# Kernel optimization log

Hardware: AMD Instinct MI355X
Metric: run time of the kernel (lower is better)

The kernel has to match this reference:

```python
import jax, jax.numpy as jnp
import numpy as np
import itertools

# LeViT-style Attention config (matches init_kwargs)
DIM = 256
KD = 32          # key_dim
H = 8            # num_heads
AR = 4           # attn_ratio
RES = 14
N = RES * RES    # 196 tokens
D = AR * KD      # per-head value dim = 128
DH = D * H       # 1024
NHKD = KD * H    # 256
HID = DH + 2 * NHKD  # 1536 = qkv width
EPS = 1e-5
SCALE = KD ** -0.5
BATCH = 256


def _bias_idxs():
    # Same construction as the torch module: index into table of unique abs offsets.
    points = list(itertools.product(range(RES), range(RES)))
    offs = {}
    idxs = []
    for p1 in points:
        for p2 in points:
            o = (abs(p1[0] - p2[0]), abs(p1[1] - p2[1]))
            if o not in offs:
                offs[o] = len(offs)
            idxs.append(offs[o])
    return np.asarray(idxs, dtype=np.int32).reshape(N, N), len(offs)


def _bn(x, g, b):
    # BatchNorm1d in training mode over the flattened (B*N, F) batch dim.
    mu = x.mean(axis=0)
    var = jnp.var(x, axis=0)  # biased, as torch BN uses for normalization
    return (x - mu) * jax.lax.rsqrt(var + EPS) * g + b


def setup_inputs() -> dict:
    key = jax.random.key(0)
    ks = jax.random.split(key, 8)
    idxs_np, n_off = _bias_idxs()  # n_off == 196 for RES=14
    x = jax.random.normal(ks[0], (BATCH, N, DIM), dtype=jnp.float32)
    Wqkv = jax.random.normal(ks[1], (HID, DIM), dtype=jnp.float32) * 0.02
    g1 = 1.0 + 0.1 * jax.random.normal(ks[2], (HID,), dtype=jnp.float32)
    b1 = 0.1 * jax.random.normal(ks[3], (HID,), dtype=jnp.float32)
    # init is zeros in the module; use small randn so the bias path is exercised
    bias_table = 0.1 * jax.random.normal(ks[4], (H, n_off), dtype=jnp.float32)
    Wproj = jax.random.normal(ks[5], (DIM, DH), dtype=jnp.float32) * 0.02
    # bn_weight_init=0 in module; use nonzero so output/grads are nontrivial
    g2 = 1.0 + 0.1 * jax.random.normal(ks[6], (DIM,), dtype=jnp.float32)
    b2 = 0.1 * jax.random.normal(ks[7], (DIM,), dtype=jnp.float32)
    return {
        "x": x, "Wqkv": Wqkv, "g1": g1, "b1": b1,
        "bias_table": bias_table, "Wproj": Wproj, "g2": g2, "b2": b2,
        "idxs": jnp.asarray(idxs_np),
    }


def reference(x, Wqkv, g1, b1, bias_table, Wproj, g2, b2, idxs):
    B, Ntok, C = x.shape
    # qkv = Linear_BN(x): bias-free linear then BN over flattened (B*N, HID)
    h = jnp.einsum('bnc,hc->bnh', x, Wqkv)
    h = _bn(h.reshape(B * Ntok, HID), g1, b1).reshape(B, Ntok, H, -1)
    q = h[..., :KD].transpose(0, 2, 1, 3)            # (B,H,N,KD)
    k = h[..., KD:2 * KD].transpose(0, 2, 1, 3)      # (B,H,N,KD)
    v = h[..., 2 * KD:].transpose(0, 2, 1, 3)        # (B,H,N,D)
    bias = bias_table[:, idxs]                       # (H,N,N) relative-position bias gather
    attn = jnp.einsum('bhnd,bhmd->bhnm', q, k) * SCALE + bias
    attn = jax.nn.softmax(attn, axis=-1)
    o = jnp.einsum('bhnm,bhmd->bhnd', attn, v)
    o = o.transpose(0, 2, 1, 3).reshape(B, Ntok, DH)
    # proj = Hardswish -> Linear_BN(dh, dim)
    o = o * jnp.clip(o + 3.0, 0.0, 6.0) / 6.0
    o = jnp.einsum('bnd,cd->bnc', o, Wproj)
    o = _bn(o.reshape(B * Ntok, C), g2, b2).reshape(B, Ntok, C)
    return o
```

## Files before the change

kernel.cpp:

```cpp
#include <hip/hip_runtime.h>

typedef _Float16 f16;
typedef __attribute__((ext_vector_type(8))) _Float16 half8;
typedef __attribute__((ext_vector_type(4))) _Float16 half4;
typedef __attribute__((ext_vector_type(4))) float   f4;

#define NTOK   196
#define MROWS  50176
#define HIDN   1536
#define HPC    192
#define DHD    1024
#define EPSV   1e-5f
#define SCALEV 0.17677669529663687f

#define GLD16(gp, lp) __builtin_amdgcn_global_load_lds( \
    (const __attribute__((address_space(1))) unsigned int*)(gp), \
    (__attribute__((address_space(3))) unsigned int*)(lp), 16, 0, 0)

__device__ inline int swz8(int row) { return (((row & 7) ^ ((row >> 3) & 7))) * 8; }

__global__ void cvt_f32_f16(const float* __restrict__ src, f16* __restrict__ dst, int n4)
{
    int i = blockIdx.x * blockDim.x + threadIdx.x;
    if (i < n4) {
        float4 v = *(const float4*)&src[i * 4];
        half4 h = { (f16)v.x, (f16)v.y, (f16)v.z, (f16)v.w };
        *(half4*)&dst[i * 4] = h;
    }
}

__global__ void build_bias(const float* __restrict__ bt, const int* __restrict__ idxs,
                           f16* __restrict__ bf)
{
    int i = blockIdx.x * 256 + threadIdx.x;
    if (i >= 8 * 208 * 224) return;
    int k = i % 224, q = (i / 224) % 208, h = i / (224 * 208);
    float v = -30000.f;
    if (q < NTOK && k < NTOK) v = bt[h * NTOK + idxs[q * NTOK + k]];
    bf[i] = (f16)v;
}

#define PIPE_BODY(CA, CB, PA, PB, ST, HASPF, GATE)                              \
  {                                                                             \
    asm volatile("s_waitcnt vmcnt(" GATE ")" ::: "memory");                     \
    __builtin_amdgcn_s_barrier();                                               \
    __builtin_amdgcn_sched_barrier(0);                                          \
    if (HASPF) {                                                                \
      const f16* Apf_ = Ab + ((ST) + 2) * 32;                                   \
      const f16* Bpf_ = Bb + ((ST) + 2) * 32;                                   \
      GLD16(Apf_,          &PA[so0]);                                           \
      GLD16(Apf_ + 16 * K, &PA[so1]);                                           \
      GLD16(Bpf_,          &PB[so0]);                                           \
      GLD16(Bpf_ + 16 * K, &PB[so1]);                                           \
    }                                                                           \
    half8 a_[4], b_[4];                                                         \
    _Pragma("unroll")                                                           \
    for (int i_ = 0; i_ < 4; ++i_) {                                            \
      a_[i_] = *(const half8*)&CA[(wm + i_ * 16 + lm) * 32 + rs];               \
      b_[i_] = *(const half8*)&CB[(wn + i_ * 16 + lm) * 32 + rs];               \
    }                                                                           \
    asm volatile("s_waitcnt lgkmcnt(0)" ::: "memory");                          \
    __builtin_amdgcn_sched_barrier(0);                                          \
    _Pragma("unroll")                                                           \
    for (int i_ = 0; i_ < 4; ++i_)                                              \
      _Pragma("unroll")                                                         \
      for (int j_ = 0; j_ < 4; ++j_)                                            \
        acc[i_][j_] = __builtin_amdgcn_mfma_f32_16x16x32_f16(                   \
            a_[i_], b_[j_], acc[i_][j_], 0, 0, 0);                              \
  }

__global__ __launch_bounds__(256) void gemm1_qkv(
    const f16* __restrict__ A, const f16* __restrict__ B,
    f16* __restrict__ C, float* __restrict__ gsum, float* __restrict__ gsq)
{
    const int K = 256, ldc = HIDN;
    __shared__ f16 As0[4096], As1[4096], As2[4096];
    __shared__ f16 Bs0[4096], Bs1[4096], Bs2[4096];
    __shared__ float ssum[128], ssq[128];

    const int t = threadIdx.x;
    const int m0 = blockIdx.x * 128, n0 = blockIdx.y * 128;
    const int wid = t >> 6, lane = t & 63, quad = lane >> 4, lm = lane & 15;
    const int wm = (wid >> 1) * 64, wn = (wid & 1) * 64;

    const int lr = lane >> 2;
    const int lc = ((lane & 3) ^ (lr & 3)) * 8;
    const int so0 = (wid * 2 + 0) * 512, so1 = (wid * 2 + 1) * 512;
    const f16* Ab = A + (long)(m0 + wid * 32 + lr) * K + lc;
    const f16* Bb = B + (long)(n0 + wid * 32 + lr) * K + lc;
    const int rs = (quad ^ (lm & 3)) * 8;

    f4 acc[4][4] = {};

    GLD16(Ab,               &As0[so0]);
    GLD16(Ab + 16 * K,      &As0[so1]);
    GLD16(Bb,               &Bs0[so0]);
    GLD16(Bb + 16 * K,      &Bs0[so1]);
    GLD16(Ab + 32,          &As1[so0]);
    GLD16(Ab + 16 * K + 32, &As1[so1]);
    GLD16(Bb + 32,          &Bs1[so0]);
    GLD16(Bb + 16 * K + 32, &Bs1[so1]);

    PIPE_BODY(As0, Bs0, As2, Bs2, 0, 1, "4");
    PIPE_BODY(As1, Bs1, As0, Bs0, 1, 1, "4");
    PIPE_BODY(As2, Bs2, As1, Bs1, 2, 1, "4");
    PIPE_BODY(As0, Bs0, As2, Bs2, 3, 1, "4");
    PIPE_BODY(As1, Bs1, As0, Bs0, 4, 1, "4");
    PIPE_BODY(As2, Bs2, As1, Bs1, 5, 1, "4");
    PIPE_BODY(As0, Bs0, As2, Bs2, 6, 0, "4");
    PIPE_BODY(As1, Bs1, As0, Bs0, 7, 0, "0");

    __syncthreads();
    if (t < 128) { ssum[t] = 0.f; ssq[t] = 0.f; }
    __syncthreads();

    #pragma unroll
    for (int j = 0; j < 4; ++j) {
        int nl = wn + j*16 + lm;
        float psum = 0.f, psq = 0.f;
        #pragma unroll
        for (int i = 0; i < 4; ++i) {
            #pragma unroll
            for (int r = 0; r < 4; ++r) {
                int ml = wm + i*16 + quad*4 + r;
                float v = acc[i][j][r];
                f16 uh = (f16)v;
                float vb = (float)uh;
                C[(long)(m0 + ml) * ldc + n0 + nl] = uh;
                psum += vb; psq += vb * vb;
            }
        }
        atomicAdd(&ssum[nl], psum);
        atomicAdd(&ssq[nl], psq);
    }
    __syncthreads();
    if (t < 128) {
        atomicAdd(&gsum[n0 + t], ssum[t]);
        atomicAdd(&gsq[n0 + t],  ssq[t]);
    }
}

__global__ __launch_bounds__(256) void gemm2_proj(
    const f16* __restrict__ A, const f16* __restrict__ B,
    float* __restrict__ C, float* __restrict__ gsum, float* __restrict__ gsq)
{
    const int K = 1024, ldc = 256;
    __shared__ f16 As0[4096], As1[4096], As2[4096];
    __shared__ f16 Bs0[4096], Bs1[4096], Bs2[4096];
    __shared__ float ssum[128], ssq[128];

    const int t = threadIdx.x;
    const int m0 = blockIdx.x * 128, n0 = blockIdx.y * 128;
    const int wid = t >> 6, lane = t & 63, quad = lane >> 4, lm = lane & 15;
    const int wm = (wid >> 1) * 64, wn = (wid & 1) * 64;

    const int lr = lane >> 2;
    const int lc = ((lane & 3) ^ (lr & 3)) * 8;
    const int so0 = (wid * 2 + 0) * 512, so1 = (wid * 2 + 1) * 512;
    const f16* Ab = A + (long)(m0 + wid * 32 + lr) * K + lc;
    const f16* Bb = B + (long)(n0 + wid * 32 + lr) * K + lc;
    const int rs = (quad ^ (lm & 3)) * 8;

    f4 acc[4][4] = {};

    GLD16(Ab,               &As0[so0]);
    GLD16(Ab + 16 * K,      &As0[so1]);
    GLD16(Bb,               &Bs0[so0]);
    GLD16(Bb + 16 * K,      &Bs0[so1]);
    GLD16(Ab + 32,          &As1[so0]);
    GLD16(Ab + 16 * K + 32, &As1[so1]);
    GLD16(Bb + 32,          &Bs1[so0]);
    GLD16(Bb + 16 * K + 32, &Bs1[so1]);

    for (int s = 0; s < 30; s += 6) {
        PIPE_BODY(As0, Bs0, As2, Bs2, s + 0, 1, "4");
        PIPE_BODY(As1, Bs1, As0, Bs0, s + 1, 1, "4");
        PIPE_BODY(As2, Bs2, As1, Bs1, s + 2, 1, "4");
        PIPE_BODY(As0, Bs0, As2, Bs2, s + 3, 1, "4");
        PIPE_BODY(As1, Bs1, As0, Bs0, s + 4, 1, "4");
        PIPE_BODY(As2, Bs2, As1, Bs1, s + 5, 1, "4");
    }
    PIPE_BODY(As0, Bs0, As2, Bs2, 30, 0, "4");
    PIPE_BODY(As1, Bs1, As0, Bs0, 31, 0, "0");

    __syncthreads();
    if (t < 128) { ssum[t] = 0.f; ssq[t] = 0.f; }
    __syncthreads();

    #pragma unroll
    for (int j = 0; j < 4; ++j) {
        int nl = wn + j*16 + lm;
        float psum = 0.f, psq = 0.f;
        #pragma unroll
        for (int i = 0; i < 4; ++i) {
            #pragma unroll
            for (int r = 0; r < 4; ++r) {
                int ml = wm + i*16 + quad*4 + r;
                float v = acc[i][j][r];
                C[(long)(m0 + ml) * ldc + n0 + nl] = v;
                psum += v; psq += v * v;
            }
        }
        atomicAdd(&ssum[nl], psum);
        atomicAdd(&ssq[nl], psq);
    }
    __syncthreads();
    if (t < 128) {
        atomicAdd(&gsum[n0 + t], ssum[t]);
        atomicAdd(&gsq[n0 + t],  ssq[t]);
    }
}

__global__ void bn_fin(const float* __restrict__ gsum, const float* __restrict__ gsq,
                       const float* __restrict__ g, const float* __restrict__ b,
                       float* __restrict__ a_out, float* __restrict__ s_out, int nch)
{
    int c = blockIdx.x * blockDim.x + threadIdx.x;
    if (c >= nch) return;
    float inv  = 1.f / (float)MROWS;
    float mean = gsum[c] * inv;
    float var  = gsq[c] * inv - mean * mean;
    float a    = g[c] * rsqrtf(var + EPSV);
    a_out[c] = a;
    s_out[c] = b[c] - mean * a;
}

__global__ __launch_bounds__(832) void attn_kernel(
    const f16* __restrict__ hbuf, const float* __restrict__ a1, const float* __restrict__ s1,
    const f16* __restrict__ bf, f16* __restrict__ obuf)
{
    __shared__ f16   ks[208][32];
    __shared__ f16   vT[128][256];
    __shared__ float af[192], sf[192];

    const int t  = threadIdx.x;
    const int bb = blockIdx.x >> 3;
    const int hh = blockIdx.x & 7;
    const int wid = t >> 6, lane = t & 63, quad = lane >> 4, lm = lane & 15;

    if (t < 192) { af[t] = a1[hh * HPC + t]; sf[t] = s1[hh * HPC + t]; }
    half8 z8 = {};
    for (int i = t; i < 4096; i += 832) *(half8*)&vT[i >> 5][(i & 31) * 8] = z8;
    if (t < 384) ks[196 + (t >> 5)][t & 31] = (f16)0.f;
    __syncthreads();

    {
        int t8 = t & 7;
        for (int rr = t >> 3; rr < NTOK; rr += 104) {
            const f16* hrow = hbuf + (long)(bb * NTOK + rr) * HIDN + hh * HPC;
            int sr = swz8(rr);
            #pragma unroll
            for (int cc = 0; cc < 3; ++cc) {
                int cb = 32 + (t8 + cc * 8) * 8;
                if (cb >= 192) continue;
                half8 raw = *(const half8*)(hrow + cb);
                if (cb < 64) {
                    half8 ov;
                    #pragma unroll
                    for (int e = 0; e < 8; ++e)
                        ov[e] = (f16)((float)raw[e] * af[cb + e] + sf[cb + e]);
                    *(half8*)&ks[rr][(cb - 32 + sr) & 31] = ov;
                } else {
                    #pragma unroll
                    for (int e = 0; e < 8; ++e) {
                        int c = cb - 64 + e;
                        f16 ov = (f16)((float)raw[e] * af[cb + e] + sf[cb + e]);
                        vT[c][(rr + swz8(c)) & 255] = ov;
                    }
                }
            }
        }
    }
    __syncthreads();

    const int mt = wid;
    const int qrow = mt * 16 + lm;
    const f16* bfh = bf + hh * 208 * 224;

    long grow = (long)bb * NTOK + qrow;
    if (grow > (long)(MROWS - 1)) grow = MROWS - 1;
    half8 qraw = *(const half8*)(hbuf + grow * HIDN + hh * HPC + quad * 8);
    half8 qf;
    #pragma unroll
    for (int e = 0; e < 8; ++e)
        qf[e] = (f16)((float)qraw[e] * af[quad * 8 + e] + sf[quad * 8 + e]);

    f4 sreg[13];
    #pragma unroll
    for (int nt = 0; nt < 13; ++nt) {
        int krow = nt * 16 + lm;
        half8 ak = *(const half8*)&ks[krow][(quad * 8 + swz8(krow)) & 31];
        f4 z = {};
        sreg[nt] = __builtin_amdgcn_mfma_f32_16x16x32_f16(ak, qf, z, 0, 0, 0);
    }

    const f16* brow = bfh + qrow * 224 + quad * 4;
    float m = -3.0e38f;
    #pragma unroll
    for (int nt = 0; nt < 13; ++nt) {
        half4 b4 = *(const half4*)(brow + nt * 16);
        #pragma unroll
        for (int r = 0; r < 4; ++r) {
            sreg[nt][r] = fmaf(sreg[nt][r], SCALEV, (float)b4[r]);
            m = fmaxf(m, sreg[nt][r]);
        }
    }
    m = fmaxf(m, __shfl_xor(m, 16));
    m = fmaxf(m, __shfl_xor(m, 32));

    float s = 0.f;
    half4 ap[13];
    #pragma unroll
    for (int nt = 0; nt < 13; ++nt) {
        float e0 = __expf(sreg[nt][0] - m);
        float e1 = __expf(sreg[nt][1] - m);
        float e2 = __expf(sreg[nt][2] - m);
        float e3 = __expf(sreg[nt][3] - m);
        s += (e0 + e1) + (e2 + e3);
        ap[nt] = half4{ (f16)e0, (f16)e1, (f16)e2, (f16)e3 };
    }
    s += __shfl_xor(s, 16);
    s += __shfl_xor(s, 32);
    float rinv = 1.f / s;

    float rv[4];
    #pragma unroll
    for (int r = 0; r < 4; ++r) rv[r] = __shfl(rinv, quad * 4 + r);

    #pragma unroll
    for (int ct = 0; ct < 8; ++ct) {
        int c = ct * 16 + lm;
        int sc = swz8(c);
        f4 oa = {};
        #pragma unroll
        for (int nt = 0; nt < 13; ++nt) {
            half4 bv = *(const half4*)&vT[c][(nt * 16 + quad * 4 + sc) & 255];
            oa = __builtin_amdgcn_mfma_f32_16x16x16f16(ap[nt], bv, oa, 0, 0, 0);
        }
        #pragma unroll
        for (int r = 0; r < 4; ++r) {
            int qr = mt * 16 + quad * 4 + r;
            if (qr < 196) {
                float v  = oa[r] * rv[r];
                float hs = v * fminf(fmaxf(v + 3.f, 0.f), 6.f) * (1.f / 6.f);
                obuf[(long)(bb * NTOK + qr) * DHD + hh * 128 + c] = (f16)hs;
            }
        }
    }
}

__global__ __launch_bounds__(256) void bn_apply(
    float* __restrict__ out, const float* __restrict__ a2, const float* __restrict__ s2)
{
    __shared__ float aL[256], sL[256];
    int t = threadIdx.x;
    aL[t] = a2[t]; sL[t] = s2[t];
    __syncthreads();
    long total = (long)MROWS * 256 / 4;
    for (long i = (long)blockIdx.x * 256 + t; i < total; i += (long)gridDim.x * 256) {
        float4 v = *(float4*)&out[i * 4];
        int cb = (int)((i * 4) & 255);
        v.x = v.x * aL[cb + 0] + sL[cb + 0];
        v.y = v.y * aL[cb + 1] + sL[cb + 1];
        v.z = v.z * aL[cb + 2] + sL[cb + 2];
        v.w = v.w * aL[cb + 3] + sL[cb + 3];
        *(float4*)&out[i * 4] = v;
    }
}

extern "C" void kernel_launch(void* const* d_in, const int* in_sizes, int n_in,
                              void* d_out, int out_size, void* d_ws, size_t ws_size,
                              hipStream_t stream)
{
    (void)in_sizes; (void)n_in; (void)out_size; (void)ws_size;
    const float* x          = (const float*)d_in[0];
    const float* Wqkv       = (const float*)d_in[1];
    const float* g1         = (const float*)d_in[2];
    const float* b1         = (const float*)d_in[3];
    const float* bias_table = (const float*)d_in[4];
    const float* Wproj      = (const float*)d_in[5];
    const float* g2         = (const float*)d_in[6];
    const float* b2         = (const float*)d_in[7];
    const int*   idxs       = (const int*)d_in[8];
    float*       out        = (float*)d_out;

    char* ws = (char*)d_ws;
    f16* hbuf = (f16*)ws;
    f16* obuf = (f16*)(ws + 154140672LL);
    f16* xh   = (f16*)(ws + 154140672LL);
    f16* wqh  = (f16*)(ws + 154140672LL + 25690112LL);
    f16* wph  = (f16*)ws;
    float* stats = (float*)(ws + 256901120LL);
    float* gsum1 = stats;            float* gsq1 = stats + 1536;
    float* gsum2 = stats + 3072;     float* gsq2 = stats + 3328;
    float* a1 = stats + 3584;        float* s1 = a1 + 1536;
    float* a2 = s1 + 1536;           float* s2 = a2 + 256;
    f16* bias_full = (f16*)(ws + 256901120LL + 65536LL);

    hipMemsetAsync(stats, 0, 3584 * sizeof(float), stream);

    cvt_f32_f16<<<12544, 256, 0, stream>>>(x, xh, 3211264);
    cvt_f32_f16<<<384,   256, 0, stream>>>(Wqkv, wqh, 98304);
    build_bias<<<1456, 256, 0, stream>>>(bias_table, idxs, bias_full);

    gemm1_qkv<<<dim3(392, 12), 256, 0, stream>>>(xh, wqh, hbuf, gsum1, gsq1);
    bn_fin<<<6, 256, 0, stream>>>(gsum1, gsq1, g1, b1, a1, s1, 1536);

    attn_kernel<<<2048, 832, 0, stream>>>(hbuf, a1, s1, bias_full, obuf);

    cvt_f32_f16<<<256, 256, 0, stream>>>(Wproj, wph, 65536);

    gemm2_proj<<<dim3(392, 2), 256, 0, stream>>>(obuf, wph, out, gsum2, gsq2);
    bn_fin<<<1, 256, 0, stream>>>(gsum2, gsq2, g2, b2, a2, s2, 256);

    bn_apply<<<1024, 256, 0, stream>>>(out, a2, s2);
}
```

Before: 440.9 us.

## Use exp2 softmax with folded log2e, packed f16 BN affine, and MFMA setprio

```diff
diff --git a/kernel.cpp b/kernel.cpp
--- a/kernel.cpp
+++ b/kernel.cpp
@@ -11,7 +11,8 @@
 #define HPC    192
 #define DHD    1024
 #define EPSV   1e-5f
-#define SCALEV 0.17677669529663687f
+#define SCALE2 0.25503524f
+#define LOG2E  1.4426950408889634f
 
 #define GLD16(gp, lp) __builtin_amdgcn_global_load_lds( \
     (const __attribute__((address_space(1))) unsigned int*)(gp), \
@@ -37,7 +38,7 @@
     int k = i % 224, q = (i / 224) % 208, h = i / (224 * 208);
     float v = -30000.f;
     if (q < NTOK && k < NTOK) v = bt[h * NTOK + idxs[q * NTOK + k]];
-    bf[i] = (f16)v;
+    bf[i] = (f16)(v * LOG2E);
 }
 
 #define PIPE_BODY(CA, CB, PA, PB, ST, HASPF, GATE)                              \
@@ -61,12 +62,14 @@
     }                                                                           \
     asm volatile("s_waitcnt lgkmcnt(0)" ::: "memory");                          \
     __builtin_amdgcn_sched_barrier(0);                                          \
+    __builtin_amdgcn_s_setprio(1);                                              \
     _Pragma("unroll")                                                           \
     for (int i_ = 0; i_ < 4; ++i_)                                              \
       _Pragma("unroll")                                                         \
       for (int j_ = 0; j_ < 4; ++j_)                                            \
         acc[i_][j_] = __builtin_amdgcn_mfma_f32_16x16x32_f16(                   \
             a_[i_], b_[j_], acc[i_][j_], 0, 0, 0);                              \
+    __builtin_amdgcn_s_setprio(0);                                              \
   }
 
 __global__ __launch_bounds__(256) void gemm1_qkv(
@@ -229,16 +232,16 @@
     const f16* __restrict__ hbuf, const float* __restrict__ a1, const float* __restrict__ s1,
     const f16* __restrict__ bf, f16* __restrict__ obuf)
 {
-    __shared__ f16   ks[208][32];
-    __shared__ f16   vT[128][256];
-    __shared__ float af[192], sf[192];
+    __shared__ f16 ks[208][32];
+    __shared__ f16 vT[128][256];
+    __shared__ f16 afh[192], sfh[192];
 
     const int t  = threadIdx.x;
     const int bb = blockIdx.x >> 3;
     const int hh = blockIdx.x & 7;
     const int wid = t >> 6, lane = t & 63, quad = lane >> 4, lm = lane & 15;
 
-    if (t < 192) { af[t] = a1[hh * HPC + t]; sf[t] = s1[hh * HPC + t]; }
+    if (t < 192) { afh[t] = (f16)a1[hh * HPC + t]; sfh[t] = (f16)s1[hh * HPC + t]; }
     half8 z8 = {};
     for (int i = t; i < 4096; i += 832) *(half8*)&vT[i >> 5][(i & 31) * 8] = z8;
     if (t < 384) ks[196 + (t >> 5)][t & 31] = (f16)0.f;
@@ -254,18 +257,16 @@
                 int cb = 32 + (t8 + cc * 8) * 8;
                 if (cb >= 192) continue;
                 half8 raw = *(const half8*)(hrow + cb);
+                half8 a8  = *(const half8*)&afh[cb];
+                half8 s8  = *(const half8*)&sfh[cb];
+                half8 ov  = raw * a8 + s8;
                 if (cb < 64) {
-                    half8 ov;
-                    #pragma unroll
-                    for (int e = 0; e < 8; ++e)
-                        ov[e] = (f16)((float)raw[e] * af[cb + e] + sf[cb + e]);
                     *(half8*)&ks[rr][(cb - 32 + sr) & 31] = ov;
                 } else {
                     #pragma unroll
                     for (int e = 0; e < 8; ++e) {
                         int c = cb - 64 + e;
-                        f16 ov = (f16)((float)raw[e] * af[cb + e] + sf[cb + e]);
-                        vT[c][(rr + swz8(c)) & 255] = ov;
+                        vT[c][(rr + swz8(c)) & 255] = ov[e];
                     }
                 }
             }
@@ -280,12 +281,12 @@
     long grow = (long)bb * NTOK + qrow;
     if (grow > (long)(MROWS - 1)) grow = MROWS - 1;
     half8 qraw = *(const half8*)(hbuf + grow * HIDN + hh * HPC + quad * 8);
-    half8 qf;
-    #pragma unroll
-    for (int e = 0; e < 8; ++e)
-        qf[e] = (f16)((float)qraw[e] * af[quad * 8 + e] + sf[quad * 8 + e]);
+    half8 qa = *(const half8*)&afh[quad * 8];
+    half8 qs = *(const half8*)&sfh[quad * 8];
+    half8 qf = qraw * qa + qs;
 
     f4 sreg[13];
+    __builtin_amdgcn_s_setprio(1);
     #pragma unroll
     for (int nt = 0; nt < 13; ++nt) {
         int krow = nt * 16 + lm;
@@ -293,6 +294,7 @@
         f4 z = {};
         sreg[nt] = __builtin_amdgcn_mfma_f32_16x16x32_f16(ak, qf, z, 0, 0, 0);
     }
+    __builtin_amdgcn_s_setprio(0);
 
     const f16* brow = bfh + qrow * 224 + quad * 4;
     float m = -3.0e38f;
@@ -301,7 +303,7 @@
         half4 b4 = *(const half4*)(brow + nt * 16);
         #pragma unroll
         for (int r = 0; r < 4; ++r) {
-            sreg[nt][r] = fmaf(sreg[nt][r], SCALEV, (float)b4[r]);
+            sreg[nt][r] = fmaf(sreg[nt][r], SCALE2, (float)b4[r]);
             m = fmaxf(m, sreg[nt][r]);
         }
     }
@@ -312,10 +314,10 @@
     half4 ap[13];
     #pragma unroll
     for (int nt = 0; nt < 13; ++nt) {
-        float e0 = __expf(sreg[nt][0] - m);
-        float e1 = __expf(sreg[nt][1] - m);
-        float e2 = __expf(sreg[nt][2] - m);
-        float e3 = __expf(sreg[nt][3] - m);
+        float e0 = exp2f(sreg[nt][0] - m);
+        float e1 = exp2f(sreg[nt][1] - m);
+        float e2 = exp2f(sreg[nt][2] - m);
+        float e3 = exp2f(sreg[nt][3] - m);
         s += (e0 + e1) + (e2 + e3);
         ap[nt] = half4{ (f16)e0, (f16)e1, (f16)e2, (f16)e3 };
     }
@@ -332,11 +334,13 @@
         int c = ct * 16 + lm;
         int sc = swz8(c);
         f4 oa = {};
+        __builtin_amdgcn_s_setprio(1);
         #pragma unroll
         for (int nt = 0; nt < 13; ++nt) {
             half4 bv = *(const half4*)&vT[c][(nt * 16 + quad * 4 + sc) & 255];
             oa = __builtin_amdgcn_mfma_f32_16x16x16f16(ap[nt], bv, oa, 0, 0, 0);
         }
+        __builtin_amdgcn_s_setprio(0);
         #pragma unroll
         for (int r = 0; r < 4; ++r) {
             int qr = mt * 16 + quad * 4 + r;
```

Result: no change. 442.1 us (+0.3%).
